# Kernel tuning notes

Hardware: AMD Instinct MI355X
Metric: run time of the kernel (lower is better)

The kernel has to match this reference:

```python
import jax, jax.numpy as jnp
import numpy as np

B, S, IN_F, OUT_F = 8, 2048, 2048, 2048
ORDER, RANK, LEAF = 3, 4, 13  # LEAF = ceil(IN_F ** (1/ORDER))


def setup_inputs() -> dict:
    key = jax.random.key(0)
    k1, k2, k3, k4 = jax.random.split(key, 4)
    inp = jax.random.normal(k1, (B, S, IN_F), dtype=jnp.float32)
    # leaf init ~ uniform(-std, std), std = gain / in_features**(1/order)
    gain = float(np.sqrt(2.0 / (1.0 + 5.0)))  # leaky_relu gain with param=sqrt(5)
    std = gain / (IN_F ** (1.0 / ORDER))
    leaf_tensor = jax.random.uniform(k2, (ORDER, RANK, LEAF, LEAF), dtype=jnp.float32,
                                     minval=-std, maxval=std)
    bound = 1.0 / np.sqrt(IN_F)
    weight = jax.random.uniform(k3, (OUT_F, IN_F), dtype=jnp.float32, minval=-bound, maxval=bound)
    bias = jax.random.uniform(k4, (OUT_F,), dtype=jnp.float32, minval=-bound, maxval=bound)
    return {"input": inp, "leaf_tensor": leaf_tensor, "weight": weight, "bias": bias}


def tensor_product_represent(leaf_tensor, out_dim, in_dim):
    order, rank, leaf, _ = leaf_tensor.shape  # static shapes
    base = leaf_tensor[0]                      # [rank, leaf, leaf]
    dim = leaf
    for i in range(1, order):                  # fixed small structural loop
        # Kronecker step: [r, d, d] x [r, l, l] -> [r, d*l, d*l]
        base = jnp.einsum('abc,ade->abdce', base, leaf_tensor[i])
        dim = dim * leaf
        base = base.reshape(rank, dim, dim)
    base = base.sum(axis=0)                    # [leaf^order, leaf^order]
    return base[:out_dim, :in_dim]


def reference(input, leaf_tensor, weight, bias):
    out_dim, in_dim = weight.shape
    delta = tensor_product_represent(leaf_tensor, out_dim, in_dim)
    w = weight + delta                          # [out, in]
    # F.linear: y = x @ w.T + b
    return jnp.einsum('bsi,oi->bso', input, w) + bias
```

## Files before the change

### kernel.cpp

```cpp
#include <hip/hip_runtime.h>
#include <hip/hip_bf16.h>
#include <stdint.h>

#define MROWS 16384
#define KDIM  2048
#define NDIM  2048
#define LEAFD 13
#define RANKD 4

typedef __bf16 bf16x8 __attribute__((ext_vector_type(8)));
typedef float  f32x4  __attribute__((ext_vector_type(4)));

__global__ void build_w_kernel(const float* __restrict__ weight,
                               const float* __restrict__ leaf,
                               __hip_bfloat16* __restrict__ wbf) {
    __shared__ float ll[3 * RANKD * LEAFD * LEAFD];
    for (int t = threadIdx.x; t < 3 * RANKD * LEAFD * LEAFD; t += blockDim.x)
        ll[t] = leaf[t];
    __syncthreads();
    int idx = blockIdx.x * blockDim.x + threadIdx.x;
    if (idx >= NDIM * KDIM) return;
    int o = idx / KDIM, i = idx % KDIM;
    int o2 = o / 169, o1 = (o / 13) % 13, o0 = o % 13;
    int i2 = i / 169, i1 = (i / 13) % 13, i0 = i % 13;
    float d = 0.f;
#pragma unroll
    for (int r = 0; r < RANKD; ++r) {
        float a = ll[( r            * LEAFD + o2) * LEAFD + i2];
        float b = ll[((RANKD   + r) * LEAFD + o1) * LEAFD + i1];
        float c = ll[((2*RANKD + r) * LEAFD + o0) * LEAFD + i0];
        d += a * b * c;
    }
    wbf[idx] = __float2bfloat16(weight[idx] + d);
}

__global__ void cvt_kernel(const float* __restrict__ x,
                           __hip_bfloat16* __restrict__ xb, int n) {
    long stride = (long)gridDim.x * blockDim.x * 8;
    for (long idx = ((long)blockIdx.x * blockDim.x + threadIdx.x) * 8; idx < n; idx += stride) {
        float4 v0 = *reinterpret_cast<const float4*>(x + idx);
        float4 v1 = *reinterpret_cast<const float4*>(x + idx + 4);
        __hip_bfloat16 tmp[8];
        tmp[0] = __float2bfloat16(v0.x); tmp[1] = __float2bfloat16(v0.y);
        tmp[2] = __float2bfloat16(v0.z); tmp[3] = __float2bfloat16(v0.w);
        tmp[4] = __float2bfloat16(v1.x); tmp[5] = __float2bfloat16(v1.y);
        tmp[6] = __float2bfloat16(v1.z); tmp[7] = __float2bfloat16(v1.w);
        *reinterpret_cast<uint4*>(xb + idx) = *reinterpret_cast<const uint4*>(tmp);
    }
}


__device__ __forceinline__ void gload16(const __hip_bfloat16* g, char* l) {
    __builtin_amdgcn_global_load_lds((const __attribute__((address_space(1))) void*)g,
                                     (__attribute__((address_space(3))) void*)l,
                                     16, 0, 0);
}

#define STAGE(base, kb, bufi, slot) do {                                          \
    gload16((base) + (kb) + gOff0, smemc + (bufi)*65536 + (slot)*16384 + lOff0);  \
    gload16((base) + (kb) + gOff1, smemc + (bufi)*65536 + (slot)*16384 + lOff1);  \
} while (0)

#define LOAD_A(mh, kk, bufc)                                                        \
    af0 = *(const bf16x8*)(smemc + (bufc)*65536 + (kk)*32768 + offA[(mh)*4+0]);     \
    af1 = *(const bf16x8*)(smemc + (bufc)*65536 + (kk)*32768 + offA[(mh)*4+1]);     \
    af2 = *(const bf16x8*)(smemc + (bufc)*65536 + (kk)*32768 + offA[(mh)*4+2]);     \
    af3 = *(const bf16x8*)(smemc + (bufc)*65536 + (kk)*32768 + offA[(mh)*4+3]);

#define LOAD_B(kk, bufc)                                                                    \
    bf0 = *(const bf16x8*)(smemc + (bufc)*65536 + (kk)*32768 + 16384 + offB[0]);            \
    bf1 = *(const bf16x8*)(smemc + (bufc)*65536 + (kk)*32768 + 16384 + offB[1]);            \
    bf2 = *(const bf16x8*)(smemc + (bufc)*65536 + (kk)*32768 + 16384 + offB[2]);            \
    bf3 = *(const bf16x8*)(smemc + (bufc)*65536 + (kk)*32768 + 16384 + offB[3]);

#define MFMA_Q(mh) do {                                                                   \
    acc[(mh)*4+0][0] = __builtin_amdgcn_mfma_f32_16x16x32_bf16(af0, bf0, acc[(mh)*4+0][0], 0,0,0); \
    acc[(mh)*4+1][0] = __builtin_amdgcn_mfma_f32_16x16x32_bf16(af1, bf0, acc[(mh)*4+1][0], 0,0,0); \
    acc[(mh)*4+2][0] = __builtin_amdgcn_mfma_f32_16x16x32_bf16(af2, bf0, acc[(mh)*4+2][0], 0,0,0); \
    acc[(mh)*4+3][0] = __builtin_amdgcn_mfma_f32_16x16x32_bf16(af3, bf0, acc[(mh)*4+3][0], 0,0,0); \
    acc[(mh)*4+0][1] = __builtin_amdgcn_mfma_f32_16x16x32_bf16(af0, bf1, acc[(mh)*4+0][1], 0,0,0); \
    acc[(mh)*4+1][1] = __builtin_amdgcn_mfma_f32_16x16x32_bf16(af1, bf1, acc[(mh)*4+1][1], 0,0,0); \
    acc[(mh)*4+2][1] = __builtin_amdgcn_mfma_f32_16x16x32_bf16(af2, bf1, acc[(mh)*4+2][1], 0,0,0); \
    acc[(mh)*4+3][1] = __builtin_amdgcn_mfma_f32_16x16x32_bf16(af3, bf1, acc[(mh)*4+3][1], 0,0,0); \
    acc[(mh)*4+0][2] = __builtin_amdgcn_mfma_f32_16x16x32_bf16(af0, bf2, acc[(mh)*4+0][2], 0,0,0); \
    acc[(mh)*4+1][2] = __builtin_amdgcn_mfma_f32_16x16x32_bf16(af1, bf2, acc[(mh)*4+1][2], 0,0,0); \
    acc[(mh)*4+2][2] = __builtin_amdgcn_mfma_f32_16x16x32_bf16(af2, bf2, acc[(mh)*4+2][2], 0,0,0); \
    acc[(mh)*4+3][2] = __builtin_amdgcn_mfma_f32_16x16x32_bf16(af3, bf2, acc[(mh)*4+3][2], 0,0,0); \
    acc[(mh)*4+0][3] = __builtin_amdgcn_mfma_f32_16x16x32_bf16(af0, bf3, acc[(mh)*4+0][3], 0,0,0); \
    acc[(mh)*4+1][3] = __builtin_amdgcn_mfma_f32_16x16x32_bf16(af1, bf3, acc[(mh)*4+1][3], 0,0,0); \
    acc[(mh)*4+2][3] = __builtin_amdgcn_mfma_f32_16x16x32_bf16(af2, bf3, acc[(mh)*4+2][3], 0,0,0); \
    acc[(mh)*4+3][3] = __builtin_amdgcn_mfma_f32_16x16x32_bf16(af3, bf3, acc[(mh)*4+3][3], 0,0,0); \
} while (0)

#define BARRIER_IN do {                                     \
    __builtin_amdgcn_sched_barrier(0);                      \
    __builtin_amdgcn_s_barrier();                           \
    asm volatile("s_waitcnt lgkmcnt(0)" ::: "memory");      \
    __builtin_amdgcn_sched_barrier(0);                      \
    __builtin_amdgcn_s_setprio(1);                          \
} while (0)

#define BARRIER_OUT do {                                    \
    __builtin_amdgcn_s_setprio(0);                          \
    __builtin_amdgcn_sched_barrier(0);                      \
    __builtin_amdgcn_s_barrier();                           \
    __builtin_amdgcn_sched_barrier(0);                      \
} while (0)

#define WAIT8 asm volatile("s_waitcnt vmcnt(8)" ::: "memory")
#define WAIT4 asm volatile("s_waitcnt vmcnt(4)" ::: "memory")
#define WAIT0 asm volatile("s_waitcnt vmcnt(0)" ::: "memory")
#define WNONE do {} while (0)

#define KTILE(t, bufc, S0, S1, S2, S3, W1, W3) do {                 \
                                                  \
    LOAD_B(0, bufc); LOAD_A(0, 0, bufc);                            \
    if (S0) STAGE(Abase, ((t)+1)*64+32, (bufc)^1, 2);               \
    BARRIER_IN; MFMA_Q(0); BARRIER_OUT;                             \
                                                  \
    LOAD_A(1, 0, bufc);                                             \
    if (S1) STAGE(Bbase, ((t)+1)*64+32, (bufc)^1, 3);               \
    W1;                                                             \
    BARRIER_IN; MFMA_Q(1); BARRIER_OUT;                             \
                                                  \
    LOAD_B(1, bufc); LOAD_A(0, 1, bufc);                            \
    if (S2) STAGE(Abase, ((t)+2)*64, (bufc), 0);                    \
    BARRIER_IN; MFMA_Q(0); BARRIER_OUT;                             \
                                                  \
    LOAD_A(1, 1, bufc);                                             \
    if (S3) STAGE(Bbase, ((t)+2)*64, (bufc), 1);                    \
    W3;                                                             \
    BARRIER_IN; MFMA_Q(1); BARRIER_OUT;                             \
} while (0)

__global__ __launch_bounds__(512, 2) void gemm8_kernel(const __hip_bfloat16* __restrict__ A,
                                                       const __hip_bfloat16* __restrict__ Wb,
                                                       const float* __restrict__ bias,
                                                       float* __restrict__ C) {
    __shared__ __align__(16) __hip_bfloat16 smem[2][4][8192];
    char* smemc = (char*)&smem[0][0][0];

    const int tid  = threadIdx.x;
    const int lane = tid & 63;
    const int wid  = tid >> 6;
    const int wr   = wid >> 2;
    const int wc   = wid & 3;

    const int bid = blockIdx.x;
    const int swz = (bid & 7) * 64 + (bid >> 3);
    const int bn  = swz >> 6;
    const int bm  = swz & 63;

    const __hip_bfloat16* Abase = A  + (size_t)bm * 256 * KDIM;
    const __hip_bfloat16* Bbase = Wb + (size_t)bn * 256 * KDIM;

    const int c0  = wid * 64 + lane;
    const int c1  = 512 + wid * 64 + lane;
    const int cs0 = c0 ^ ((c0 >> 3) & 7);
    const int cs1 = c1 ^ ((c1 >> 3) & 7);
    const int gOff0 = (cs0 >> 2) * KDIM + (cs0 & 3) * 8;
    const int gOff1 = (cs1 >> 2) * KDIM + (cs1 & 3) * 8;
    const int lOff0 = wid * 1024;
    const int lOff1 = 8192 + wid * 1024;

    const int rsel = lane & 15;
    const int kby  = (lane >> 4) * 16;
    int offA[8], offB[4];
#pragma unroll
    for (int m = 0; m < 8; ++m) {
        int a = (wr * 128 + m * 16 + rsel) * 64 + kby;
        offA[m] = a ^ (((a >> 7) & 7) << 4);
    }
#pragma unroll
    for (int n = 0; n < 4; ++n) {
        int a = (wc * 64 + n * 16 + rsel) * 64 + kby;
        offB[n] = a ^ (((a >> 7) & 7) << 4);
    }

    f32x4 acc[8][4];
#pragma unroll
    for (int m = 0; m < 8; ++m)
#pragma unroll
        for (int n = 0; n < 4; ++n)
            acc[m][n] = (f32x4){0.f, 0.f, 0.f, 0.f};

    bf16x8 af0, af1, af2, af3, bf0, bf1, bf2, bf3;

    STAGE(Abase,  0, 0, 0);
    STAGE(Bbase,  0, 0, 1);
    STAGE(Abase, 32, 0, 2);
    STAGE(Bbase, 32, 0, 3);
    STAGE(Abase, 64, 1, 0);
    STAGE(Bbase, 64, 1, 1);
    WAIT8;
    __builtin_amdgcn_sched_barrier(0);
    __builtin_amdgcn_s_barrier();
    __builtin_amdgcn_sched_barrier(0);

    for (int tt = 0; tt < 30; tt += 2) {
        KTILE(tt,     0, 1, 1, 1, 1, WAIT8, WAIT8);
        KTILE(tt + 1, 1, 1, 1, 1, 1, WAIT8, WAIT8);
    }
    KTILE(30, 0, 1, 1, 0, 0, WAIT8, WAIT4);
    KTILE(31, 1, 0, 0, 0, 0, WAIT0, WNONE);

    const int col0 = lane & 15;
    const int r0   = (lane >> 4) * 4;
#pragma unroll
    for (int n = 0; n < 4; ++n) {
        const int cg = bn * 256 + wc * 64 + n * 16 + col0;
        const float bv = bias[cg];
#pragma unroll
        for (int m = 0; m < 8; ++m) {
            const size_t rg = (size_t)bm * 256 + wr * 128 + m * 16 + r0;
#pragma unroll
            for (int r = 0; r < 4; ++r)
                C[(rg + r) * NDIM + cg] = acc[m][n][r] + bv;
        }
    }
}

__global__ void naive_kernel(const float* __restrict__ x,
                             const float* __restrict__ leaf,
                             const float* __restrict__ W,
                             const float* __restrict__ bias,
                             float* __restrict__ out) {
    long idx = (long)blockIdx.x * blockDim.x + threadIdx.x;
    if (idx >= (long)MROWS * NDIM) return;
    int  o = (int)(idx % NDIM);
    long m = idx / NDIM;
    int o2 = o / 169, o1 = (o / 13) % 13, o0 = o % 13;
    float acc = 0.f;
    for (int i = 0; i < KDIM; ++i) {
        int i2 = i / 169, i1 = (i / 13) % 13, i0 = i % 13;
        float d = 0.f;
#pragma unroll
        for (int r = 0; r < RANKD; ++r)
            d += leaf[( r     * LEAFD + o2) * LEAFD + i2]
               * leaf[((4 + r) * LEAFD + o1) * LEAFD + i1]
               * leaf[((8 + r) * LEAFD + o0) * LEAFD + i0];
        acc += x[m * KDIM + i] * (W[(long)o * KDIM + i] + d);
    }
    out[idx] = acc + bias[o];
}

extern "C" void kernel_launch(void* const* d_in, const int* in_sizes, int n_in,
                              void* d_out, int out_size, void* d_ws, size_t ws_size,
                              hipStream_t stream) {
    const float* x      = (const float*)d_in[0];
    const float* leaf   = (const float*)d_in[1];
    const float* weight = (const float*)d_in[2];
    const float* bias   = (const float*)d_in[3];
    float* out = (float*)d_out;

    const size_t needA = (size_t)MROWS * KDIM * sizeof(__hip_bfloat16);
    const size_t needW = (size_t)NDIM  * KDIM * sizeof(__hip_bfloat16);

    if (ws_size >= needA + needW) {
        __hip_bfloat16* xb = (__hip_bfloat16*)d_ws;
        __hip_bfloat16* wb = (__hip_bfloat16*)((char*)d_ws + needA);
        build_w_kernel<<<(NDIM * KDIM + 255) / 256, 256, 0, stream>>>(weight, leaf, wb);
        cvt_kernel<<<2048, 256, 0, stream>>>(x, xb, MROWS * KDIM);
        gemm8_kernel<<<(MROWS / 256) * (NDIM / 256), 512, 0, stream>>>(xb, wb, bias, out);
    } else {
        long total = (long)MROWS * NDIM;
        naive_kernel<<<(int)((total + 255) / 256), 256, 0, stream>>>(x, leaf, weight, bias, out);
    }
}
```

Before: 206.9 us.

## Process two M tiles per workgroup with cross-tile prefetch and 256-block grid

Each workgroup now computes two consecutive 256-row output tiles that share the same W column block. The grid shrinks from 512 to 256 blocks, and the staging pipeline runs straight across the tile boundary, so the next tile's A loads are prefetched during the first tile's tail. The wait depth drops from vmcnt(8) to vmcnt(4). The goal is to cut pipeline prologue/epilogue cost and the tail effect of a second wave, in exchange for a single wave of longer blocks and the first tile's epilogue stores stalling the pipeline.

After: 209.6 us. Within noise of the previous version (+1.3%).

```diff
diff --git a/kernel.cpp b/kernel.cpp
--- a/kernel.cpp
+++ b/kernel.cpp
@@ -107,38 +107,51 @@
     __builtin_amdgcn_sched_barrier(0);                      \
 } while (0)
 
-#define WAIT8 asm volatile("s_waitcnt vmcnt(8)" ::: "memory")
 #define WAIT4 asm volatile("s_waitcnt vmcnt(4)" ::: "memory")
 #define WAIT0 asm volatile("s_waitcnt vmcnt(0)" ::: "memory")
 #define WNONE do {} while (0)
 
-#define KTILE(t, bufc, S0, S1, S2, S3, W1, W3) do {                 \
-                                                  \
-    LOAD_B(0, bufc); LOAD_A(0, 0, bufc);                            \
-    if (S0) STAGE(Abase, ((t)+1)*64+32, (bufc)^1, 2);               \
+#define KTILEM(BC, AP1, K1, AP2, K2, S0, S1, S2, S3, W3) do {       \
+                                                            \
+    LOAD_B(0, BC); LOAD_A(0, 0, BC);                                \
+    if (S0) STAGE(AP1, (K1)+32, (BC)^1, 2);                         \
     BARRIER_IN; MFMA_Q(0); BARRIER_OUT;                             \
-                                                  \
-    LOAD_A(1, 0, bufc);                                             \
-    if (S1) STAGE(Bbase, ((t)+1)*64+32, (bufc)^1, 3);               \
-    W1;                                                             \
+                                                            \
+    LOAD_A(1, 0, BC);                                               \
+    if (S1) STAGE(Bbase, (K1)+32, (BC)^1, 3);                       \
     BARRIER_IN; MFMA_Q(1); BARRIER_OUT;                             \
-                                                  \
-    LOAD_B(1, bufc); LOAD_A(0, 1, bufc);                            \
-    if (S2) STAGE(Abase, ((t)+2)*64, (bufc), 0);                    \
+                                                            \
+    LOAD_B(1, BC); LOAD_A(0, 1, BC);                                \
+    if (S2) STAGE(AP2, (K2), (BC), 0);                              \
     BARRIER_IN; MFMA_Q(0); BARRIER_OUT;                             \
-                                                  \
-    LOAD_A(1, 1, bufc);                                             \
-    if (S3) STAGE(Bbase, ((t)+2)*64, (bufc), 1);                    \
+                                                            \
+    LOAD_A(1, 1, BC);                                               \
+    if (S3) STAGE(Bbase, (K2), (BC), 1);                            \
     W3;                                                             \
     BARRIER_IN; MFMA_Q(1); BARRIER_OUT;                             \
 } while (0)
 
-__global__ __launch_bounds__(512, 2) void gemm8_kernel(const __hip_bfloat16* __restrict__ A,
-                                                       const __hip_bfloat16* __restrict__ Wb,
-                                                       const float* __restrict__ bias,
-                                                       float* __restrict__ C) {
+#define EPILOG(ROWBASE) do {                                                    \
+    _Pragma("unroll")                                                           \
+    for (int n = 0; n < 4; ++n) {                                               \
+        const int cg = bn * 256 + wc * 64 + n * 16 + col0;                      \
+        const float bv = bias[cg];                                              \
+        _Pragma("unroll")                                                       \
+        for (int m = 0; m < 8; ++m) {                                           \
+            const size_t rg = (size_t)(ROWBASE) + wr * 128 + m * 16 + r0;       \
+            _Pragma("unroll")                                                   \
+            for (int r = 0; r < 4; ++r)                                         \
+                C[(rg + r) * NDIM + cg] = acc[m][n][r] + bv;                    \
+        }                                                                       \
+    }                                                                           \
+} while (0)
+
+__global__ __launch_bounds__(512, 2) void gemm11_kernel(const __hip_bfloat16* __restrict__ A,
+                                                        const __hip_bfloat16* __restrict__ Wb,
+                                                        const float* __restrict__ bias,
+                                                        float* __restrict__ C) {
     __shared__ __align__(16) __hip_bfloat16 smem[2][4][8192];
-    char* smemc = (char*)&smem[0][0][0];
+    char* smemc = (char*)smem;
 
     const int tid  = threadIdx.x;
     const int lane = tid & 63;
@@ -147,15 +160,16 @@
     const int wc   = wid & 3;
 
     const int bid = blockIdx.x;
-    const int swz = (bid & 7) * 64 + (bid >> 3);
-    const int bn  = swz >> 6;
-    const int bm  = swz & 63;
-
-    const __hip_bfloat16* Abase = A  + (size_t)bm * 256 * KDIM;
-    const __hip_bfloat16* Bbase = Wb + (size_t)bn * 256 * KDIM;
+    const int swz = (bid & 7) * 32 + (bid >> 3);
+    const int bn  = swz >> 5;
+    const int q   = swz & 31;
+
+    const __hip_bfloat16* Abase0 = A + (size_t)(q * 2) * 256 * KDIM;
+    const __hip_bfloat16* Abase1 = Abase0 + (size_t)256 * KDIM;
+    const __hip_bfloat16* Bbase  = Wb + (size_t)bn * 256 * KDIM;
 
     const int c0  = wid * 64 + lane;
-    const int c1  = 512 + wid * 64 + lane;
+    const int c1  = 512 + c0;
     const int cs0 = c0 ^ ((c0 >> 3) & 7);
     const int cs1 = c1 ^ ((c1 >> 3) & 7);
     const int gOff0 = (cs0 >> 2) * KDIM + (cs0 & 3) * 8;
@@ -186,38 +200,42 @@
 
     bf16x8 af0, af1, af2, af3, bf0, bf1, bf2, bf3;
 
-    STAGE(Abase,  0, 0, 0);
-    STAGE(Bbase,  0, 0, 1);
-    STAGE(Abase, 32, 0, 2);
-    STAGE(Bbase, 32, 0, 3);
-    STAGE(Abase, 64, 1, 0);
-    STAGE(Bbase, 64, 1, 1);
-    WAIT8;
+    const int col0 = lane & 15;
+    const int r0   = (lane >> 4) * 4;
+
+    STAGE(Abase0,  0, 0, 0);
+    STAGE(Bbase,   0, 0, 1);
+    STAGE(Abase0, 32, 0, 2);
+    STAGE(Bbase,  32, 0, 3);
+    STAGE(Abase0, 64, 1, 0);
+    STAGE(Bbase,  64, 1, 1);
+    WAIT4;
     __builtin_amdgcn_sched_barrier(0);
     __builtin_amdgcn_s_barrier();
     __builtin_amdgcn_sched_barrier(0);
 
-    for (int tt = 0; tt < 30; tt += 2) {
-        KTILE(tt,     0, 1, 1, 1, 1, WAIT8, WAIT8);
-        KTILE(tt + 1, 1, 1, 1, 1, 1, WAIT8, WAIT8);
-    }
-    KTILE(30, 0, 1, 1, 0, 0, WAIT8, WAIT4);
-    KTILE(31, 1, 0, 0, 0, 0, WAIT0, WNONE);
-
-    const int col0 = lane & 15;
-    const int r0   = (lane >> 4) * 4;
-#pragma unroll
-    for (int n = 0; n < 4; ++n) {
-        const int cg = bn * 256 + wc * 64 + n * 16 + col0;
-        const float bv = bias[cg];
-#pragma unroll
-        for (int m = 0; m < 8; ++m) {
-            const size_t rg = (size_t)bm * 256 + wr * 128 + m * 16 + r0;
-#pragma unroll
-            for (int r = 0; r < 4; ++r)
-                C[(rg + r) * NDIM + cg] = acc[m][n][r] + bv;
-        }
-    }
+    for (int t = 0; t < 30; t += 2) {
+        KTILEM(0, Abase0, (t+1)*64, Abase0, (t+2)*64, 1, 1, 1, 1, WAIT4);
+        KTILEM(1, Abase0, (t+2)*64, Abase0, (t+3)*64, 1, 1, 1, 1, WAIT4);
+    }
+    KTILEM(0, Abase0, 31*64, Abase1, 0, 1, 1, 1, 1, WAIT4);
+    KTILEM(1, Abase1, 0, Abase1, 64, 1, 1, 1, 1, WAIT4);
+
+    EPILOG((size_t)(q * 2) * 256);
+#pragma unroll
+    for (int m = 0; m < 8; ++m)
+#pragma unroll
+        for (int n = 0; n < 4; ++n)
+            acc[m][n] = (f32x4){0.f, 0.f, 0.f, 0.f};
+
+    for (int t = 32; t < 62; t += 2) {
+        KTILEM(0, Abase1, (t-31)*64, Abase1, (t-30)*64, 1, 1, 1, 1, WAIT4);
+        KTILEM(1, Abase1, (t-30)*64, Abase1, (t-29)*64, 1, 1, 1, 1, WAIT4);
+    }
+    KTILEM(0, Abase1, 31*64, Abase1, 0, 1, 1, 0, 0, WAIT0);
+    KTILEM(1, Abase1, 0, Abase1, 0, 0, 0, 0, 0, WNONE);
+
+    EPILOG((size_t)(q * 2 + 1) * 256);
 }
 
 __global__ void naive_kernel(const float* __restrict__ x,
@@ -261,7 +279,7 @@
         __hip_bfloat16* wb = (__hip_bfloat16*)((char*)d_ws + needA);
         build_w_kernel<<<(NDIM * KDIM + 255) / 256, 256, 0, stream>>>(weight, leaf, wb);
         cvt_kernel<<<2048, 256, 0, stream>>>(x, xb, MROWS * KDIM);
-        gemm8_kernel<<<(MROWS / 256) * (NDIM / 256), 512, 0, stream>>>(xb, wb, bias, out);
+        gemm11_kernel<<<256, 512, 0, stream>>>(xb, wb, bias, out);
     } else {
         long total = (long)MROWS * NDIM;
         naive_kernel<<<(int)((total + 255) / 256), 256, 0, stream>>>(x, leaf, weight, bias, out);
```

## Merge prep kernels and simplify GEMM k-loop to one barrier per tile

Applied to the files above, without the earlier changes.

The weight-build and input-conversion kernels are merged into one prep launch that splits work by block index. The GEMM main loop drops the staged 4-phase scheme, which had 8 barriers per k-tile plus partial vmcnt waits. It now prefetches the whole next tile into the other buffer at the start of each span, runs all MFMA quarters with priority toggling, then does one vmcnt(0) wait and one barrier. Launch bounds drop to one block per SIMD-group, which frees registers but may reduce the latency hiding that came from a second resident block and from finer-grained overlap.

New measurement: 207.6 us. No clear change (+0.4%).

```diff
diff --git a/kernel.cpp b/kernel.cpp
--- a/kernel.cpp
+++ b/kernel.cpp
@@ -11,41 +11,43 @@
 typedef __bf16 bf16x8 __attribute__((ext_vector_type(8)));
 typedef float  f32x4  __attribute__((ext_vector_type(4)));
 
-__global__ void build_w_kernel(const float* __restrict__ weight,
-                               const float* __restrict__ leaf,
-                               __hip_bfloat16* __restrict__ wbf) {
-    __shared__ float ll[3 * RANKD * LEAFD * LEAFD];
-    for (int t = threadIdx.x; t < 3 * RANKD * LEAFD * LEAFD; t += blockDim.x)
-        ll[t] = leaf[t];
-    __syncthreads();
-    int idx = blockIdx.x * blockDim.x + threadIdx.x;
-    if (idx >= NDIM * KDIM) return;
-    int o = idx / KDIM, i = idx % KDIM;
-    int o2 = o / 169, o1 = (o / 13) % 13, o0 = o % 13;
-    int i2 = i / 169, i1 = (i / 13) % 13, i0 = i % 13;
-    float d = 0.f;
-#pragma unroll
-    for (int r = 0; r < RANKD; ++r) {
-        float a = ll[( r            * LEAFD + o2) * LEAFD + i2];
-        float b = ll[((RANKD   + r) * LEAFD + o1) * LEAFD + i1];
-        float c = ll[((2*RANKD + r) * LEAFD + o0) * LEAFD + i0];
-        d += a * b * c;
-    }
-    wbf[idx] = __float2bfloat16(weight[idx] + d);
-}
-
-__global__ void cvt_kernel(const float* __restrict__ x,
-                           __hip_bfloat16* __restrict__ xb, int n) {
-    long stride = (long)gridDim.x * blockDim.x * 8;
-    for (long idx = ((long)blockIdx.x * blockDim.x + threadIdx.x) * 8; idx < n; idx += stride) {
-        float4 v0 = *reinterpret_cast<const float4*>(x + idx);
-        float4 v1 = *reinterpret_cast<const float4*>(x + idx + 4);
-        __hip_bfloat16 tmp[8];
-        tmp[0] = __float2bfloat16(v0.x); tmp[1] = __float2bfloat16(v0.y);
-        tmp[2] = __float2bfloat16(v0.z); tmp[3] = __float2bfloat16(v0.w);
-        tmp[4] = __float2bfloat16(v1.x); tmp[5] = __float2bfloat16(v1.y);
-        tmp[6] = __float2bfloat16(v1.z); tmp[7] = __float2bfloat16(v1.w);
-        *reinterpret_cast<uint4*>(xb + idx) = *reinterpret_cast<const uint4*>(tmp);
+__global__ void prep_kernel(const float* __restrict__ x,
+                            const float* __restrict__ leaf,
+                            const float* __restrict__ weight,
+                            __hip_bfloat16* __restrict__ xb,
+                            __hip_bfloat16* __restrict__ wbf) {
+    const int bid = blockIdx.x;
+    if (bid < 16384) {
+        __shared__ float ll[3 * RANKD * LEAFD * LEAFD];
+        for (int t = threadIdx.x; t < 3 * RANKD * LEAFD * LEAFD; t += blockDim.x)
+            ll[t] = leaf[t];
+        __syncthreads();
+        int idx = bid * 256 + threadIdx.x;
+        int o = idx / KDIM, i = idx % KDIM;
+        int o2 = o / 169, o1 = (o / 13) % 13, o0 = o % 13;
+        int i2 = i / 169, i1 = (i / 13) % 13, i0 = i % 13;
+        float d = 0.f;
+#pragma unroll
+        for (int r = 0; r < RANKD; ++r) {
+            float a = ll[( r            * LEAFD + o2) * LEAFD + i2];
+            float b = ll[((RANKD   + r) * LEAFD + o1) * LEAFD + i1];
+            float c = ll[((2*RANKD + r) * LEAFD + o0) * LEAFD + i0];
+            d += a * b * c;
+        }
+        wbf[idx] = __float2bfloat16(weight[idx] + d);
+    } else {
+        const long n = (long)MROWS * KDIM;
+        const long stride = (long)2048 * 256 * 8;
+        for (long idx = ((long)(bid - 16384) * 256 + threadIdx.x) * 8; idx < n; idx += stride) {
+            float4 v0 = *reinterpret_cast<const float4*>(x + idx);
+            float4 v1 = *reinterpret_cast<const float4*>(x + idx + 4);
+            __hip_bfloat16 tmp[8];
+            tmp[0] = __float2bfloat16(v0.x); tmp[1] = __float2bfloat16(v0.y);
+            tmp[2] = __float2bfloat16(v0.z); tmp[3] = __float2bfloat16(v0.w);
+            tmp[4] = __float2bfloat16(v1.x); tmp[5] = __float2bfloat16(v1.y);
+            tmp[6] = __float2bfloat16(v1.z); tmp[7] = __float2bfloat16(v1.w);
+            *reinterpret_cast<uint4*>(xb + idx) = *reinterpret_cast<const uint4*>(tmp);
+        }
     }
 }
 
@@ -92,53 +94,42 @@
     acc[(mh)*4+3][3] = __builtin_amdgcn_mfma_f32_16x16x32_bf16(af3, bf3, acc[(mh)*4+3][3], 0,0,0); \
 } while (0)
 
-#define BARRIER_IN do {                                     \
-    __builtin_amdgcn_sched_barrier(0);                      \
-    __builtin_amdgcn_s_barrier();                           \
-    asm volatile("s_waitcnt lgkmcnt(0)" ::: "memory");      \
-    __builtin_amdgcn_sched_barrier(0);                      \
-    __builtin_amdgcn_s_setprio(1);                          \
+#define W0 asm volatile("s_waitcnt vmcnt(0)" ::: "memory")
+#define WN do {} while (0)
+
+#define SPAN(t, BC, SG, WT) do {                                    \
+    if (SG) {                                                       \
+        STAGE(Abase, ((t)+1)*64,      (BC)^1, 0);                   \
+        STAGE(Bbase, ((t)+1)*64,      (BC)^1, 1);                   \
+        STAGE(Abase, ((t)+1)*64 + 32, (BC)^1, 2);                   \
+        STAGE(Bbase, ((t)+1)*64 + 32, (BC)^1, 3);                   \
+    }                                                               \
+    LOAD_B(0, BC); LOAD_A(0, 0, BC);                                \
+    __builtin_amdgcn_s_setprio(1);                                  \
+    MFMA_Q(0);                                                      \
+    __builtin_amdgcn_s_setprio(0);                                  \
+    LOAD_A(1, 0, BC);                                               \
+    __builtin_amdgcn_s_setprio(1);                                  \
+    MFMA_Q(1);                                                      \
+    __builtin_amdgcn_s_setprio(0);                                  \
+    LOAD_B(1, BC); LOAD_A(0, 1, BC);                                \
+    __builtin_amdgcn_s_setprio(1);                                  \
+    MFMA_Q(0);                                                      \
+    __builtin_amdgcn_s_setprio(0);                                  \
+    LOAD_A(1, 1, BC);                                               \
+    __builtin_amdgcn_s_setprio(1);                                  \
+    MFMA_Q(1);                                                      \
+    __builtin_amdgcn_s_setprio(0);                                  \
+    WT;                                                             \
+    __builtin_amdgcn_s_barrier();                                   \
 } while (0)
 
-#define BARRIER_OUT do {                                    \
-    __builtin_amdgcn_s_setprio(0);                          \
-    __builtin_amdgcn_sched_barrier(0);                      \
-    __builtin_amdgcn_s_barrier();                           \
-    __builtin_amdgcn_sched_barrier(0);                      \
-} while (0)
-
-#define WAIT8 asm volatile("s_waitcnt vmcnt(8)" ::: "memory")
-#define WAIT4 asm volatile("s_waitcnt vmcnt(4)" ::: "memory")
-#define WAIT0 asm volatile("s_waitcnt vmcnt(0)" ::: "memory")
-#define WNONE do {} while (0)
-
-#define KTILE(t, bufc, S0, S1, S2, S3, W1, W3) do {                 \
-                                                  \
-    LOAD_B(0, bufc); LOAD_A(0, 0, bufc);                            \
-    if (S0) STAGE(Abase, ((t)+1)*64+32, (bufc)^1, 2);               \
-    BARRIER_IN; MFMA_Q(0); BARRIER_OUT;                             \
-                                                  \
-    LOAD_A(1, 0, bufc);                                             \
-    if (S1) STAGE(Bbase, ((t)+1)*64+32, (bufc)^1, 3);               \
-    W1;                                                             \
-    BARRIER_IN; MFMA_Q(1); BARRIER_OUT;                             \
-                                                  \
-    LOAD_B(1, bufc); LOAD_A(0, 1, bufc);                            \
-    if (S2) STAGE(Abase, ((t)+2)*64, (bufc), 0);                    \
-    BARRIER_IN; MFMA_Q(0); BARRIER_OUT;                             \
-                                                  \
-    LOAD_A(1, 1, bufc);                                             \
-    if (S3) STAGE(Bbase, ((t)+2)*64, (bufc), 1);                    \
-    W3;                                                             \
-    BARRIER_IN; MFMA_Q(1); BARRIER_OUT;                             \
-} while (0)
-
-__global__ __launch_bounds__(512, 2) void gemm8_kernel(const __hip_bfloat16* __restrict__ A,
-                                                       const __hip_bfloat16* __restrict__ Wb,
-                                                       const float* __restrict__ bias,
-                                                       float* __restrict__ C) {
+__global__ __launch_bounds__(512, 1) void gemm12_kernel(const __hip_bfloat16* __restrict__ A,
+                                                        const __hip_bfloat16* __restrict__ Wb,
+                                                        const float* __restrict__ bias,
+                                                        float* __restrict__ C) {
     __shared__ __align__(16) __hip_bfloat16 smem[2][4][8192];
-    char* smemc = (char*)&smem[0][0][0];
+    char* smemc = (char*)smem;
 
     const int tid  = threadIdx.x;
     const int lane = tid & 63;
@@ -155,7 +146,7 @@
     const __hip_bfloat16* Bbase = Wb + (size_t)bn * 256 * KDIM;
 
     const int c0  = wid * 64 + lane;
-    const int c1  = 512 + wid * 64 + lane;
+    const int c1  = 512 + c0;
     const int cs0 = c0 ^ ((c0 >> 3) & 7);
     const int cs1 = c1 ^ ((c1 >> 3) & 7);
     const int gOff0 = (cs0 >> 2) * KDIM + (cs0 & 3) * 8;
@@ -190,19 +181,15 @@
     STAGE(Bbase,  0, 0, 1);
     STAGE(Abase, 32, 0, 2);
     STAGE(Bbase, 32, 0, 3);
-    STAGE(Abase, 64, 1, 0);
-    STAGE(Bbase, 64, 1, 1);
-    WAIT8;
-    __builtin_amdgcn_sched_barrier(0);
+    W0;
     __builtin_amdgcn_s_barrier();
-    __builtin_amdgcn_sched_barrier(0);
-
-    for (int tt = 0; tt < 30; tt += 2) {
-        KTILE(tt,     0, 1, 1, 1, 1, WAIT8, WAIT8);
-        KTILE(tt + 1, 1, 1, 1, 1, 1, WAIT8, WAIT8);
-    }
-    KTILE(30, 0, 1, 1, 0, 0, WAIT8, WAIT4);
-    KTILE(31, 1, 0, 0, 0, 0, WAIT0, WNONE);
+
+    for (int t = 0; t < 30; t += 2) {
+        SPAN(t,     0, 1, W0);
+        SPAN(t + 1, 1, 1, W0);
+    }
+    SPAN(30, 0, 1, W0);
+    SPAN(31, 1, 0, WN);
 
     const int col0 = lane & 15;
     const int r0   = (lane >> 4) * 4;
@@ -259,9 +246,8 @@
     if (ws_size >= needA + needW) {
         __hip_bfloat16* xb = (__hip_bfloat16*)d_ws;
         __hip_bfloat16* wb = (__hip_bfloat16*)((char*)d_ws + needA);
-        build_w_kernel<<<(NDIM * KDIM + 255) / 256, 256, 0, stream>>>(weight, leaf, wb);
-        cvt_kernel<<<2048, 256, 0, stream>>>(x, xb, MROWS * KDIM);
-        gemm8_kernel<<<(MROWS / 256) * (NDIM / 256), 512, 0, stream>>>(xb, wb, bias, out);
+        prep_kernel<<<16384 + 2048, 256, 0, stream>>>(x, leaf, weight, xb, wb);
+        gemm12_kernel<<<(MROWS / 256) * (NDIM / 256), 512, 0, stream>>>(xb, wb, bias, out);
     } else {
         long total = (long)MROWS * NDIM;
         naive_kernel<<<(int)((total + 255) / 256), 256, 0, stream>>>(x, leaf, weight, bias, out);
```

## Merge prep kernels into one launch and relax GEMM vmcnt waits

Applied to the files above, without the earlier changes.

The separate weight-build and input-conversion kernels become a single prep kernel that picks its role from the block index, saving one launch and letting both jobs run at the same time. The GEMM main loop also drops the mid-tile vmcnt wait and waits only once per half-tile at vmcnt(4) instead of vmcnt(8), which changes how much prefetch overlap the pipeline keeps. Waiting for fewer outstanding loads in one place could expose more memory latency, while removing a wait point could add scheduling freedom. Correctness depends on the new wait counts still covering the LDS buffers read next.

After: 202.4 us. 1.02x faster.

```diff
diff --git a/kernel.cpp b/kernel.cpp
--- a/kernel.cpp
+++ b/kernel.cpp
@@ -11,41 +11,43 @@
 typedef __bf16 bf16x8 __attribute__((ext_vector_type(8)));
 typedef float  f32x4  __attribute__((ext_vector_type(4)));
 
-__global__ void build_w_kernel(const float* __restrict__ weight,
-                               const float* __restrict__ leaf,
-                               __hip_bfloat16* __restrict__ wbf) {
-    __shared__ float ll[3 * RANKD * LEAFD * LEAFD];
-    for (int t = threadIdx.x; t < 3 * RANKD * LEAFD * LEAFD; t += blockDim.x)
-        ll[t] = leaf[t];
-    __syncthreads();
-    int idx = blockIdx.x * blockDim.x + threadIdx.x;
-    if (idx >= NDIM * KDIM) return;
-    int o = idx / KDIM, i = idx % KDIM;
-    int o2 = o / 169, o1 = (o / 13) % 13, o0 = o % 13;
-    int i2 = i / 169, i1 = (i / 13) % 13, i0 = i % 13;
-    float d = 0.f;
-#pragma unroll
-    for (int r = 0; r < RANKD; ++r) {
-        float a = ll[( r            * LEAFD + o2) * LEAFD + i2];
-        float b = ll[((RANKD   + r) * LEAFD + o1) * LEAFD + i1];
-        float c = ll[((2*RANKD + r) * LEAFD + o0) * LEAFD + i0];
-        d += a * b * c;
-    }
-    wbf[idx] = __float2bfloat16(weight[idx] + d);
-}
-
-__global__ void cvt_kernel(const float* __restrict__ x,
-                           __hip_bfloat16* __restrict__ xb, int n) {
-    long stride = (long)gridDim.x * blockDim.x * 8;
-    for (long idx = ((long)blockIdx.x * blockDim.x + threadIdx.x) * 8; idx < n; idx += stride) {
-        float4 v0 = *reinterpret_cast<const float4*>(x + idx);
-        float4 v1 = *reinterpret_cast<const float4*>(x + idx + 4);
-        __hip_bfloat16 tmp[8];
-        tmp[0] = __float2bfloat16(v0.x); tmp[1] = __float2bfloat16(v0.y);
-        tmp[2] = __float2bfloat16(v0.z); tmp[3] = __float2bfloat16(v0.w);
-        tmp[4] = __float2bfloat16(v1.x); tmp[5] = __float2bfloat16(v1.y);
-        tmp[6] = __float2bfloat16(v1.z); tmp[7] = __float2bfloat16(v1.w);
-        *reinterpret_cast<uint4*>(xb + idx) = *reinterpret_cast<const uint4*>(tmp);
+__global__ void prep_kernel(const float* __restrict__ x,
+                            const float* __restrict__ leaf,
+                            const float* __restrict__ weight,
+                            __hip_bfloat16* __restrict__ xb,
+                            __hip_bfloat16* __restrict__ wbf) {
+    const int bid = blockIdx.x;
+    if (bid < 2048) {
+        const long n = (long)MROWS * KDIM;
+        const long stride = (long)2048 * 256 * 8;
+        for (long idx = ((long)bid * 256 + threadIdx.x) * 8; idx < n; idx += stride) {
+            float4 v0 = *reinterpret_cast<const float4*>(x + idx);
+            float4 v1 = *reinterpret_cast<const float4*>(x + idx + 4);
+            __hip_bfloat16 tmp[8];
+            tmp[0] = __float2bfloat16(v0.x); tmp[1] = __float2bfloat16(v0.y);
+            tmp[2] = __float2bfloat16(v0.z); tmp[3] = __float2bfloat16(v0.w);
+            tmp[4] = __float2bfloat16(v1.x); tmp[5] = __float2bfloat16(v1.y);
+            tmp[6] = __float2bfloat16(v1.z); tmp[7] = __float2bfloat16(v1.w);
+            *reinterpret_cast<uint4*>(xb + idx) = *reinterpret_cast<const uint4*>(tmp);
+        }
+    } else {
+        __shared__ float ll[3 * RANKD * LEAFD * LEAFD];
+        for (int t = threadIdx.x; t < 3 * RANKD * LEAFD * LEAFD; t += blockDim.x)
+            ll[t] = leaf[t];
+        __syncthreads();
+        int idx = (bid - 2048) * 256 + threadIdx.x;
+        int o = idx / KDIM, i = idx % KDIM;
+        int o2 = o / 169, o1 = (o / 13) % 13, o0 = o % 13;
+        int i2 = i / 169, i1 = (i / 13) % 13, i0 = i % 13;
+        float d = 0.f;
+#pragma unroll
+        for (int r = 0; r < RANKD; ++r) {
+            float a = ll[( r            * LEAFD + o2) * LEAFD + i2];
+            float b = ll[((RANKD   + r) * LEAFD + o1) * LEAFD + i1];
+            float c = ll[((2*RANKD + r) * LEAFD + o0) * LEAFD + i0];
+            d += a * b * c;
+        }
+        wbf[idx] = __float2bfloat16(weight[idx] + d);
     }
 }
 
@@ -107,12 +109,11 @@
     __builtin_amdgcn_sched_barrier(0);                      \
 } while (0)
 
-#define WAIT8 asm volatile("s_waitcnt vmcnt(8)" ::: "memory")
 #define WAIT4 asm volatile("s_waitcnt vmcnt(4)" ::: "memory")
 #define WAIT0 asm volatile("s_waitcnt vmcnt(0)" ::: "memory")
 #define WNONE do {} while (0)
 
-#define KTILE(t, bufc, S0, S1, S2, S3, W1, W3) do {                 \
+#define KTILE(t, bufc, S0, S1, S2, S3, W3) do {                     \
                                                   \
     LOAD_B(0, bufc); LOAD_A(0, 0, bufc);                            \
     if (S0) STAGE(Abase, ((t)+1)*64+32, (bufc)^1, 2);               \
@@ -120,7 +121,6 @@
                                                   \
     LOAD_A(1, 0, bufc);                                             \
     if (S1) STAGE(Bbase, ((t)+1)*64+32, (bufc)^1, 3);               \
-    W1;                                                             \
     BARRIER_IN; MFMA_Q(1); BARRIER_OUT;                             \
                                                   \
     LOAD_B(1, bufc); LOAD_A(0, 1, bufc);                            \
@@ -192,17 +192,17 @@
     STAGE(Bbase, 32, 0, 3);
     STAGE(Abase, 64, 1, 0);
     STAGE(Bbase, 64, 1, 1);
-    WAIT8;
+    WAIT4;
     __builtin_amdgcn_sched_barrier(0);
     __builtin_amdgcn_s_barrier();
     __builtin_amdgcn_sched_barrier(0);
 
     for (int tt = 0; tt < 30; tt += 2) {
-        KTILE(tt,     0, 1, 1, 1, 1, WAIT8, WAIT8);
-        KTILE(tt + 1, 1, 1, 1, 1, 1, WAIT8, WAIT8);
-    }
-    KTILE(30, 0, 1, 1, 0, 0, WAIT8, WAIT4);
-    KTILE(31, 1, 0, 0, 0, 0, WAIT0, WNONE);
+        KTILE(tt,     0, 1, 1, 1, 1, WAIT4);
+        KTILE(tt + 1, 1, 1, 1, 1, 1, WAIT4);
+    }
+    KTILE(30, 0, 1, 1, 0, 0, WAIT0);
+    KTILE(31, 1, 0, 0, 0, 0, WNONE);
 
     const int col0 = lane & 15;
     const int r0   = (lane >> 4) * 4;
@@ -259,8 +259,7 @@
     if (ws_size >= needA + needW) {
         __hip_bfloat16* xb = (__hip_bfloat16*)d_ws;
         __hip_bfloat16* wb = (__hip_bfloat16*)((char*)d_ws + needA);
-        build_w_kernel<<<(NDIM * KDIM + 255) / 256, 256, 0, stream>>>(weight, leaf, wb);
-        cvt_kernel<<<2048, 256, 0, stream>>>(x, xb, MROWS * KDIM);
+        prep_kernel<<<2048 + 16384, 256, 0, stream>>>(x, leaf, weight, xb, wb);
         gemm8_kernel<<<(MROWS / 256) * (NDIM / 256), 512, 0, stream>>>(xb, wb, bias, out);
     } else {
         long total = (long)MROWS * NDIM;
```
